# Kernel tuning notes

Measured on AMD Instinct MI355X. Metric: run time of the kernel, lower is better.

The kernel has to match this reference:

```python
import jax, jax.numpy as jnp
import numpy as np
import math

H = 16  # n_heads


def setup_inputs() -> dict:
    key = jax.random.key(0)
    ks = jax.random.split(key, 12)
    B, S, D = 8, 1024, 1024
    inp = {
        "query": jax.random.normal(ks[0], (B, S, D), jnp.float32),
        "key_": jax.random.normal(ks[1], (B, S, D), jnp.float32),
        "value": jax.random.normal(ks[2], (B, S, D), jnp.float32),
        "mask": jnp.ones((B, S, S), jnp.int32),
        "attn_pos": jax.random.normal(ks[3], (1, H, S, S), jnp.float32),
    }
    sc = 1.0 / math.sqrt(D)
    for i, nm in enumerate(["q", "k", "v", "o"]):
        inp[f"w{nm}"] = jax.random.normal(ks[4 + i], (D, D), jnp.float32) * sc
        inp[f"b{nm}"] = jax.random.normal(ks[8 + i], (D,), jnp.float32) * 0.01
    return inp


def reference(query, key_, value, mask, attn_pos, wq, bq, wk, bk, wv, bv, wo, bo):
    B, S, D = query.shape
    dk = D // H

    def proj(x, w, b):  # [B,S,D] -> [B,H,S,dk]
        return (x @ w.T + b).reshape(B, S, H, dk).transpose(0, 2, 1, 3)

    q = proj(query, wq, bq)
    k = proj(key_, wk, bk)
    v = proj(value, wv, bv)

    # attn_pos branch: scale by sqrt(2*d_k), add positional bias
    scores = jnp.einsum("bhqd,bhkd->bhqk", q, k) / math.sqrt(2 * dk) + attn_pos
    scores = jnp.where(mask[:, None] == 0, -1e9, scores)
    p = jax.nn.softmax(scores, axis=-1)  # dropout inactive (eval)
    x = jnp.einsum("bhqk,bhkd->bhqd", p, v)
    x = x.transpose(0, 2, 1, 3).reshape(B, S, D)
    x = x @ wo.T + bo          # linears[-1] applied once...
    return x @ wo.T + bo       # ...and again, faithful to source
```

## Files before the change

### kernel.cpp

```cpp
#include <hip/hip_runtime.h>
#include <hip/hip_bf16.h>

typedef unsigned short u16;
typedef unsigned int u32;
typedef __attribute__((ext_vector_type(8))) short bfrag;
typedef __attribute__((ext_vector_type(4))) float f32x4;

#define DEVINL __device__ __forceinline__

DEVINL u16 f2bf(float f) {
  u32 u = __float_as_uint(f);
  u32 r = (u + 0x7fffu + ((u >> 16) & 1u)) >> 16;
  return (u16)r;
}
DEVINL float bf2f(u16 u) { return __uint_as_float(((u32)u) << 16); }
DEVINL u32 cvtpk(float lo, float hi) {
  u32 r;
  asm("v_cvt_pk_bf16_f32 %0, %1, %2" : "=v"(r) : "v"(lo), "v"(hi));
  return r;
}
DEVINL u16 f2bf_hw(float v) { return (u16)cvtpk(v, v); }
DEVINL float fmax3(float a, float b, float c) { return fmaxf(fmaxf(a, b), c); }

DEVINL void gload_lds16(const void* g, void* l) {
  __builtin_amdgcn_global_load_lds(
      (const __attribute__((address_space(1))) void*)g,
      (__attribute__((address_space(3))) void*)l, 16, 0, 0);
}

DEVINL void storeC(u16* C, size_t idx, float v) { C[idx] = f2bf_hw(v); }
DEVINL void storeC(float* C, size_t idx, float v) { C[idx] = v; }

#define SBAR0 __builtin_amdgcn_sched_barrier(0)


__global__ void cast_v4(const float* __restrict__ in, u16* __restrict__ out, int n4, float s) {
  const int i = blockIdx.x * 256 + threadIdx.x;
  if (i < n4) {
    const float4 f = ((const float4*)in)[i];
    uint2 r;
    r.x = cvtpk(f.x * s, f.y * s);
    r.y = cvtpk(f.z * s, f.w * s);
    ((uint2*)out)[i] = r;
  }
}

__global__ void pack_mask(const int* __restrict__ mask, u32* __restrict__ bits) {
  const size_t wi = (size_t)blockIdx.x * 256 + threadIdx.x;
  const int* src = mask + wi * 32;
  u32 v = 0;
#pragma unroll
  for (int i = 0; i < 8; ++i) {
    const int4 m4 = ((const int4*)src)[i];
    if (m4.x) v |= 1u << (i * 4 + 0);
    if (m4.y) v |= 1u << (i * 4 + 1);
    if (m4.z) v |= 1u << (i * 4 + 2);
    if (m4.w) v |= 1u << (i * 4 + 3);
  }
  bits[wi] = v;
}

__global__ void transpose_cast(const float* __restrict__ in, u16* __restrict__ out) {
  __shared__ u16 tile[64][65];
  const int t = threadIdx.x;
  const int bx = blockIdx.x, by = blockIdx.y;
#pragma unroll
  for (int p = 0; p < 4; ++p) {
    const int r = (t >> 4) + p * 16;
    const int c = (t & 15) * 4;
    const float4 f = *(const float4*)&in[(size_t)(by * 64 + r) * 1024 + bx * 64 + c];
    tile[c + 0][r] = f2bf(f.x);
    tile[c + 1][r] = f2bf(f.y);
    tile[c + 2][r] = f2bf(f.z);
    tile[c + 3][r] = f2bf(f.w);
  }
  __syncthreads();
#pragma unroll
  for (int p = 0; p < 4; ++p) {
    const int r = (t >> 4) + p * 16;
    const int c = (t & 15) * 4;
    uint2 v;
    v.x = (u32)tile[r][c] | ((u32)tile[r][c + 1] << 16);
    v.y = (u32)tile[r][c + 2] | ((u32)tile[r][c + 3] << 16);
    *(uint2*)&out[(size_t)(bx * 64 + r) * 1024 + by * 64 + c] = v;
  }
}

__global__ void bias2(const float* __restrict__ wo, const float* __restrict__ bo,
                      float* __restrict__ bo2) {
  const int w = threadIdx.x >> 6, lane = threadIdx.x & 63;
  const int row = blockIdx.x * 4 + w;
  const float* src = wo + (size_t)row * 1024;
  float s = 0.f;
#pragma unroll
  for (int i = 0; i < 4; ++i) {
    const float4 f = *(const float4*)&src[lane * 4 + i * 256];
    const float4 g = *(const float4*)&bo[lane * 4 + i * 256];
    s += f.x * g.x + f.y * g.y + f.z * g.z + f.w * g.w;
  }
#pragma unroll
  for (int d = 1; d < 64; d <<= 1) s += __shfl_xor(s, d);
  if (lane == 0) bo2[row] = s + bo[row];
}

__global__ __launch_bounds__(256) void gemm_bt_64(
    const u16* __restrict__ A, const u16* __restrict__ W,
    u16* __restrict__ C, int N, int K) {
  __shared__ u16 sA[64 * 64];
  __shared__ u16 sB[64 * 64];
  const int t = threadIdx.x;
  const int w = t >> 6, lane = t & 63;
  const int lr = lane & 15, lk = (lane >> 4) * 8;
  const int m0 = blockIdx.x * 64, n0 = blockIdx.y * 64;
  f32x4 acc[4] = {};
  for (int k0 = 0; k0 < K; k0 += 64) {
#pragma unroll
    for (int i = 0; i < 2; ++i) {
      const int idx = i * 256 + t;
      const int row = idx >> 3;
      const int col = (idx & 7) * 8;
      gload_lds16(A + (size_t)(m0 + row) * K + k0 + col, &sA[idx * 8]);
      gload_lds16(W + (size_t)(n0 + row) * K + k0 + col, &sB[idx * 8]);
    }
    __syncthreads();
#pragma unroll
    for (int ks = 0; ks < 2; ++ks) {
      const bfrag av = *(const bfrag*)&sA[(w * 16 + lr) * 64 + ks * 32 + lk];
#pragma unroll
      for (int n = 0; n < 4; ++n) {
        const bfrag bv = *(const bfrag*)&sB[(n * 16 + lr) * 64 + ks * 32 + lk];
        acc[n] = __builtin_amdgcn_mfma_f32_16x16x32_bf16(av, bv, acc[n], 0, 0, 0);
      }
    }
    __syncthreads();
  }
  const int orow = (lane >> 4) * 4;
#pragma unroll
  for (int n = 0; n < 4; ++n)
#pragma unroll
    for (int j = 0; j < 4; ++j)
      C[(size_t)(m0 + w * 16 + orow + j) * N + n0 + n * 16 + lr] = f2bf_hw(acc[n][j]);
}


template <typename OutT>
__global__ __launch_bounds__(256) void gemm_bt_a16(
    const u16* __restrict__ A, const u16* __restrict__ W,
    const float* __restrict__ bias, OutT* __restrict__ C,
    int M, int N, int K) {
  __shared__ __align__(16) u16 sA[2][128 * 64];
  __shared__ __align__(16) u16 sB[2][128 * 64];
  const int t = threadIdx.x;
  const int w = t >> 6, lane = t & 63;
  const int lr = lane & 15, lg = lane >> 4;
  const int m0 = blockIdx.x * 128, n0 = blockIdx.y * 128;
  const int wr = (w >> 1) * 64, wc = (w & 1) * 64;
  f32x4 acc[4][4] = {};
  const int nk = K >> 6;

#pragma unroll
  for (int i = 0; i < 4; ++i) {
    const int idx = i * 256 + t;
    const int row = idx >> 3;
    const int col = ((idx & 7) ^ (row & 7)) * 8;
    gload_lds16(A + (size_t)(m0 + row) * K + col, (char*)sA[0] + idx * 16);
    gload_lds16(W + (size_t)(n0 + row) * K + col, (char*)sB[0] + idx * 16);
  }
  SBAR0; asm volatile("s_waitcnt vmcnt(0)" ::: "memory"); SBAR0;
  __builtin_amdgcn_s_barrier(); SBAR0;

#pragma unroll 2
  for (int kt = 0; kt < nk; ++kt) {
    const int cur = kt & 1;
    if (kt < nk - 1) {
      const int k0 = (kt + 1) * 64;
#pragma unroll
      for (int i = 0; i < 4; ++i) {
        const int idx = i * 256 + t;
        const int row = idx >> 3;
        const int col = ((idx & 7) ^ (row & 7)) * 8;
        gload_lds16(A + (size_t)(m0 + row) * K + k0 + col, (char*)sA[cur ^ 1] + idx * 16);
        gload_lds16(W + (size_t)(n0 + row) * K + k0 + col, (char*)sB[cur ^ 1] + idx * 16);
      }
    }
    const char* pA = (const char*)sA[cur];
    const char* pB = (const char*)sB[cur];
#pragma unroll
    for (int ks = 0; ks < 2; ++ks) {
      bfrag av[4], bv[4];
#pragma unroll
      for (int m = 0; m < 4; ++m) {
        const int row = wr + m * 16 + lr;
        av[m] = *(const bfrag*)(pA + row * 128 + ((ks * 64 + lg * 16) ^ ((row & 7) << 4)));
      }
#pragma unroll
      for (int n = 0; n < 4; ++n) {
        const int row = wc + n * 16 + lr;
        bv[n] = *(const bfrag*)(pB + row * 128 + ((ks * 64 + lg * 16) ^ ((row & 7) << 4)));
      }
#pragma unroll
      for (int m = 0; m < 4; ++m)
#pragma unroll
        for (int n = 0; n < 4; ++n)
          acc[m][n] = __builtin_amdgcn_mfma_f32_16x16x32_bf16(av[m], bv[n], acc[m][n], 0, 0, 0);
    }
    if (kt < nk - 1) {
      SBAR0; asm volatile("s_waitcnt vmcnt(0)" ::: "memory"); SBAR0;
      __builtin_amdgcn_s_barrier(); SBAR0;
    }
  }

  float bz[4];
#pragma unroll
  for (int n = 0; n < 4; ++n) bz[n] = bias[n0 + wc + n * 16 + lr];
  const int orow = lg * 4;
#pragma unroll
  for (int m = 0; m < 4; ++m) {
#pragma unroll
    for (int n = 0; n < 4; ++n) {
      const int r = m0 + wr + m * 16 + orow;
      const int c = n0 + wc + n * 16 + lr;
#pragma unroll
      for (int j = 0; j < 4; ++j)
        storeC(C, (size_t)(r + j) * N + c, acc[m][n][j] + bz[n]);
    }
  }
}

template <typename OutT>
__global__ __launch_bounds__(256) void gemm_bt_a32(
    const float* __restrict__ A, const u16* __restrict__ W,
    const float* __restrict__ bias, OutT* __restrict__ C,
    int M, int N, int K, float oscale) {
  __shared__ __align__(16) u16 sA[2][128 * 64];
  __shared__ __align__(16) u16 sB[2][128 * 64];
  const int t = threadIdx.x;
  const int w = t >> 6, lane = t & 63;
  const int lr = lane & 15, lg = lane >> 4;
  const int m0 = blockIdx.x * 128, n0 = blockIdx.y * 128;
  const int wr = (w >> 1) * 64, wc = (w & 1) * 64;
  f32x4 acc[4][4] = {};
  const int nk = K >> 6;

#pragma unroll
  for (int i = 0; i < 4; ++i) {
    const int idx = i * 256 + t;
    const int row = idx >> 3;
    const int cg = idx & 7;
    const float* src = A + (size_t)(m0 + row) * K + cg * 8;
    const f32x4 f0 = *(const f32x4*)src;
    const f32x4 f1 = *(const f32x4*)(src + 4);
    uint4 pk;
    pk.x = cvtpk(f0[0], f0[1]);
    pk.y = cvtpk(f0[2], f0[3]);
    pk.z = cvtpk(f1[0], f1[1]);
    pk.w = cvtpk(f1[2], f1[3]);
    *(uint4*)((char*)sA[0] + row * 128 + ((cg ^ (row & 7)) * 16)) = pk;
    gload_lds16(W + (size_t)(n0 + row) * K + ((cg ^ (row & 7)) * 8), (char*)sB[0] + idx * 16);
  }
  SBAR0; asm volatile("s_waitcnt vmcnt(0) lgkmcnt(0)" ::: "memory"); SBAR0;
  __builtin_amdgcn_s_barrier(); SBAR0;

#pragma unroll 2
  for (int kt = 0; kt < nk; ++kt) {
    const int cur = kt & 1;
    f32x4 fa[4][2];
    if (kt < nk - 1) {
      const int k0 = (kt + 1) * 64;
#pragma unroll
      for (int i = 0; i < 4; ++i) {
        const int idx = i * 256 + t;
        const int row = idx >> 3;
        const int cg = idx & 7;
        const float* src = A + (size_t)(m0 + row) * K + k0 + cg * 8;
        fa[i][0] = *(const f32x4*)src;
        fa[i][1] = *(const f32x4*)(src + 4);
      }
#pragma unroll
      for (int i = 0; i < 4; ++i) {
        const int idx = i * 256 + t;
        const int row = idx >> 3;
        const int cg = idx & 7;
        gload_lds16(W + (size_t)(n0 + row) * K + k0 + ((cg ^ (row & 7)) * 8),
                    (char*)sB[cur ^ 1] + idx * 16);
      }
    }
    const char* pA = (const char*)sA[cur];
    const char* pB = (const char*)sB[cur];
#pragma unroll
    for (int ks = 0; ks < 2; ++ks) {
      bfrag av[4], bv[4];
#pragma unroll
      for (int m = 0; m < 4; ++m) {
        const int row = wr + m * 16 + lr;
        av[m] = *(const bfrag*)(pA + row * 128 + ((ks * 64 + lg * 16) ^ ((row & 7) << 4)));
      }
#pragma unroll
      for (int n = 0; n < 4; ++n) {
        const int row = wc + n * 16 + lr;
        bv[n] = *(const bfrag*)(pB + row * 128 + ((ks * 64 + lg * 16) ^ ((row & 7) << 4)));
      }
#pragma unroll
      for (int m = 0; m < 4; ++m)
#pragma unroll
        for (int n = 0; n < 4; ++n)
          acc[m][n] = __builtin_amdgcn_mfma_f32_16x16x32_bf16(av[m], bv[n], acc[m][n], 0, 0, 0);
    }
    if (kt < nk - 1) {
#pragma unroll
      for (int i = 0; i < 4; ++i) {
        const int idx = i * 256 + t;
        const int row = idx >> 3;
        const int cg = idx & 7;
        uint4 pk;
        pk.x = cvtpk(fa[i][0][0], fa[i][0][1]);
        pk.y = cvtpk(fa[i][0][2], fa[i][0][3]);
        pk.z = cvtpk(fa[i][1][0], fa[i][1][1]);
        pk.w = cvtpk(fa[i][1][2], fa[i][1][3]);
        *(uint4*)((char*)sA[cur ^ 1] + row * 128 + ((cg ^ (row & 7)) * 16)) = pk;
      }
      SBAR0; asm volatile("s_waitcnt vmcnt(0) lgkmcnt(0)" ::: "memory"); SBAR0;
      __builtin_amdgcn_s_barrier(); SBAR0;
    }
  }

  float bz[4];
#pragma unroll
  for (int n = 0; n < 4; ++n) bz[n] = bias[n0 + wc + n * 16 + lr];
  const int orow = lg * 4;
#pragma unroll
  for (int m = 0; m < 4; ++m) {
#pragma unroll
    for (int n = 0; n < 4; ++n) {
      const int r = m0 + wr + m * 16 + orow;
      const int c = n0 + wc + n * 16 + lr;
#pragma unroll
      for (int j = 0; j < 4; ++j)
        storeC(C, (size_t)(r + j) * N + c, (acc[m][n][j] + bz[n]) * oscale);
    }
  }
}

__global__ __launch_bounds__(256) void gemm_bt_a32_vt(
    const float* __restrict__ A, const u16* __restrict__ W,
    const float* __restrict__ bias, u16* __restrict__ Vt,
    int M, int N, int K) {
  __shared__ __align__(16) u16 sA[2][128 * 64];
  __shared__ __align__(16) u16 sB[2][128 * 64];
  const int t = threadIdx.x;
  const int w = t >> 6, lane = t & 63;
  const int lr = lane & 15, lg = lane >> 4;
  const int m0 = blockIdx.x * 128, n0 = blockIdx.y * 128;
  const int wr = (w >> 1) * 64, wc = (w & 1) * 64;
  f32x4 acc[4][4] = {};
  const int nk = K >> 6;

#pragma unroll
  for (int i = 0; i < 4; ++i) {
    const int idx = i * 256 + t;
    const int row = idx >> 3;
    const int cg = idx & 7;
    const float* src = A + (size_t)(m0 + row) * K + cg * 8;
    const f32x4 f0 = *(const f32x4*)src;
    const f32x4 f1 = *(const f32x4*)(src + 4);
    uint4 pk;
    pk.x = cvtpk(f0[0], f0[1]);
    pk.y = cvtpk(f0[2], f0[3]);
    pk.z = cvtpk(f1[0], f1[1]);
    pk.w = cvtpk(f1[2], f1[3]);
    *(uint4*)((char*)sA[0] + row * 128 + ((cg ^ (row & 7)) * 16)) = pk;
    gload_lds16(W + (size_t)(n0 + row) * K + ((cg ^ (row & 7)) * 8), (char*)sB[0] + idx * 16);
  }
  SBAR0; asm volatile("s_waitcnt vmcnt(0) lgkmcnt(0)" ::: "memory"); SBAR0;
  __builtin_amdgcn_s_barrier(); SBAR0;

#pragma unroll 2
  for (int kt = 0; kt < nk; ++kt) {
    const int cur = kt & 1;
    f32x4 fa[4][2];
    if (kt < nk - 1) {
      const int k0 = (kt + 1) * 64;
#pragma unroll
      for (int i = 0; i < 4; ++i) {
        const int idx = i * 256 + t;
        const int row = idx >> 3;
        const int cg = idx & 7;
        const float* src = A + (size_t)(m0 + row) * K + k0 + cg * 8;
        fa[i][0] = *(const f32x4*)src;
        fa[i][1] = *(const f32x4*)(src + 4);
      }
#pragma unroll
      for (int i = 0; i < 4; ++i) {
        const int idx = i * 256 + t;
        const int row = idx >> 3;
        const int cg = idx & 7;
        gload_lds16(W + (size_t)(n0 + row) * K + k0 + ((cg ^ (row & 7)) * 8),
                    (char*)sB[cur ^ 1] + idx * 16);
      }
    }
    const char* pA = (const char*)sA[cur];
    const char* pB = (const char*)sB[cur];
#pragma unroll
    for (int ks = 0; ks < 2; ++ks) {
      bfrag av[4], bv[4];
#pragma unroll
      for (int m = 0; m < 4; ++m) {
        const int row = wr + m * 16 + lr;
        av[m] = *(const bfrag*)(pA + row * 128 + ((ks * 64 + lg * 16) ^ ((row & 7) << 4)));
      }
#pragma unroll
      for (int n = 0; n < 4; ++n) {
        const int row = wc + n * 16 + lr;
        bv[n] = *(const bfrag*)(pB + row * 128 + ((ks * 64 + lg * 16) ^ ((row & 7) << 4)));
      }
#pragma unroll
      for (int m = 0; m < 4; ++m)
#pragma unroll
        for (int n = 0; n < 4; ++n)
          acc[m][n] = __builtin_amdgcn_mfma_f32_16x16x32_bf16(av[m], bv[n], acc[m][n], 0, 0, 0);
    }
    if (kt < nk - 1) {
#pragma unroll
      for (int i = 0; i < 4; ++i) {
        const int idx = i * 256 + t;
        const int row = idx >> 3;
        const int cg = idx & 7;
        uint4 pk;
        pk.x = cvtpk(fa[i][0][0], fa[i][0][1]);
        pk.y = cvtpk(fa[i][0][2], fa[i][0][3]);
        pk.z = cvtpk(fa[i][1][0], fa[i][1][1]);
        pk.w = cvtpk(fa[i][1][2], fa[i][1][3]);
        *(uint4*)((char*)sA[cur ^ 1] + row * 128 + ((cg ^ (row & 7)) * 16)) = pk;
      }
      SBAR0; asm volatile("s_waitcnt vmcnt(0) lgkmcnt(0)" ::: "memory"); SBAR0;
      __builtin_amdgcn_s_barrier(); SBAR0;
    }
  }

  float bz[4];
#pragma unroll
  for (int n = 0; n < 4; ++n) bz[n] = bias[n0 + wc + n * 16 + lr];
  const int orow = lg * 4;
#pragma unroll
  for (int m = 0; m < 4; ++m) {
#pragma unroll
    for (int n = 0; n < 4; ++n) {
      const int r0 = m0 + wr + m * 16 + orow;
      const int c = n0 + wc + n * 16 + lr;
      const int bb = r0 >> 10, s = r0 & 1023;
      const int h = c >> 6, d = c & 63;
      uint2 v;
      v.x = cvtpk(acc[m][n][0] + bz[n], acc[m][n][1] + bz[n]);
      v.y = cvtpk(acc[m][n][2] + bz[n], acc[m][n][3] + bz[n]);
      *(uint2*)&Vt[(((size_t)bb * 16 + h) * 64 + d) * 1024 + s] = v;
    }
  }
}


__global__ __launch_bounds__(512, 4) void attn_fwd(
    const u16* __restrict__ Qm, const u16* __restrict__ Km,
    const u16* __restrict__ Vt, const float* __restrict__ pos,
    const u32* __restrict__ mbits, u16* __restrict__ Om) {
  const int bb = blockIdx.x >> 3;
  const int qt = blockIdx.x & 7;
  const int h = blockIdx.y;
  const int t = threadIdx.x;
  const int w = t >> 6, lane = t & 63;
  const int lr = lane & 15, lg = lane >> 4;
  const float log2e = 1.4426950408889634f;

  __shared__ __align__(16) char smem[81920];

  const int q0 = qt * 128;
  const size_t baseQ = ((size_t)bb * 1024) * 1024 + (size_t)h * 64;
  const size_t baseV = ((size_t)(bb * 16 + h) * 64) * 1024;
  const int qg = q0 + w * 16 + lr;
  const float* posrow = pos + ((size_t)h * 1024 + qg) * 1024;
  const u32* mrow = mbits + ((size_t)bb * 1024 + qg) * 32;
  const int sr = t >> 3, sw8 = t & 7;
  const int scol = (sw8 ^ (sr & 7)) * 8;

#pragma unroll
  for (int i = 0; i < 2; ++i) {
    const int idx = i * 512 + t;
    const int r = idx >> 3;
    gload_lds16(Qm + baseQ + (size_t)(q0 + r) * 1024 + ((idx & 7) ^ (r & 7)) * 8, smem + idx * 16);
  }
  gload_lds16(Km + baseQ + (size_t)sr * 1024 + scol, smem + 16384 + t * 16);
  gload_lds16(Vt + baseV + (size_t)sr * 1024 + scol, smem + 40960 + t * 16);
  gload_lds16(Km + baseQ + (size_t)(64 + sr) * 1024 + scol, smem + 24576 + t * 16);
  gload_lds16(Vt + baseV + (size_t)sr * 1024 + 64 + scol, smem + 49152 + t * 16);

  uint4 mraw[8];
#pragma unroll
  for (int i = 0; i < 8; ++i) mraw[i] = *(const uint4*)&mrow[i * 4];
  float4 pz[4];
#pragma unroll
  for (int n = 0; n < 4; ++n) pz[n] = *(const float4*)&posrow[n * 16 + lg * 4];

  u32 ok = 0xffffffffu;
#pragma unroll
  for (int i = 0; i < 8; ++i) ok &= mraw[i].x & mraw[i].y & mraw[i].z & mraw[i].w;
  const bool allone = __all(ok == 0xffffffffu);

  SBAR0; asm volatile("s_waitcnt vmcnt(4)" ::: "memory"); SBAR0;
  __builtin_amdgcn_s_barrier(); SBAR0;

  bfrag qv[2];
#pragma unroll
  for (int ks = 0; ks < 2; ++ks) {
    const int byt = (w * 16 + lr) * 128 + ((ks * 64 + lg * 16) ^ ((lr & 7) << 4));
    qv[ks] = *(const bfrag*)(smem + byt);
  }

  f32x4 o[4] = {};
  float m_q = -3.0e38f, l_q = 0.f;
  char* pbuf = smem + 65536 + w * 2048;

#pragma unroll
  for (int kt = 0; kt < 16; ++kt) {
    const int cb = kt % 3;
    const char* sK = smem + 16384 + cb * 8192;
    const char* sV = smem + 40960 + cb * 8192;

    if (kt < 14) {
      const int kn = (kt + 2) * 64;
      const int db = (kt + 2) % 3;
      gload_lds16(Km + baseQ + (size_t)(kn + sr) * 1024 + scol, smem + 16384 + db * 8192 + t * 16);
      gload_lds16(Vt + baseV + (size_t)sr * 1024 + kn + scol, smem + 40960 + db * 8192 + t * 16);
    }
    float4 pzn[4];
    if (kt < 15) {
      const int kn = (kt + 1) * 64;
#pragma unroll
      for (int n = 0; n < 4; ++n) pzn[n] = *(const float4*)&posrow[kn + n * 16 + lg * 4];
    }

    f32x4 s[4] = {};
    __builtin_amdgcn_s_setprio(1);
#pragma unroll
    for (int ks = 0; ks < 2; ++ks) {
#pragma unroll
      for (int n = 0; n < 4; ++n) {
        const int byt = (n * 16 + lr) * 128 + ((ks * 64 + lg * 16) ^ ((lr & 7) << 4));
        const bfrag kf = *(const bfrag*)(sK + byt);
        s[n] = __builtin_amdgcn_mfma_f32_16x16x32_bf16(kf, qv[ks], s[n], 0, 0, 0);
      }
    }
    __builtin_amdgcn_s_setprio(0);

    float pv[16];
#pragma unroll
    for (int n = 0; n < 4; ++n) {
      pv[n * 4 + 0] = fmaf(pz[n].x, log2e, s[n][0]);
      pv[n * 4 + 1] = fmaf(pz[n].y, log2e, s[n][1]);
      pv[n * 4 + 2] = fmaf(pz[n].z, log2e, s[n][2]);
      pv[n * 4 + 3] = fmaf(pz[n].w, log2e, s[n][3]);
    }

    if (!allone) {
      const u32 a0 = mrow[kt * 2], a1 = mrow[kt * 2 + 1];
#pragma unroll
      for (int n = 0; n < 4; ++n)
#pragma unroll
        for (int j = 0; j < 4; ++j) {
          const int kl = n * 16 + lg * 4 + j;
          const u32 mw = (kl & 32) ? a1 : a0;
          if (!((mw >> (kl & 31)) & 1u)) pv[n * 4 + j] = -1.0e9f;
        }
    }

    float tmax = fmax3(pv[0], pv[1], pv[2]);
    tmax = fmax3(tmax, pv[3], pv[4]);
    tmax = fmax3(tmax, pv[5], pv[6]);
    tmax = fmax3(tmax, pv[7], pv[8]);
    tmax = fmax3(tmax, pv[9], pv[10]);
    tmax = fmax3(tmax, pv[11], pv[12]);
    tmax = fmax3(tmax, pv[13], pv[14]);
    tmax = fmaxf(tmax, pv[15]);
    tmax = fmaxf(tmax, __shfl_xor(tmax, 16));
    tmax = fmaxf(tmax, __shfl_xor(tmax, 32));

    if (!__all(tmax <= m_q + 8.0f)) {
      const float mn = fmaxf(m_q, tmax);
      const float sc = __builtin_amdgcn_exp2f(m_q - mn);
      l_q *= sc;
#pragma unroll
      for (int j = 0; j < 4; ++j) {
        const float scj = __shfl(sc, lg * 4 + j);
#pragma unroll
        for (int n = 0; n < 4; ++n) o[n][j] *= scj;
      }
      m_q = mn;
    }
    float rs = 0.f;
#pragma unroll
    for (int i2 = 0; i2 < 16; ++i2) {
      pv[i2] = __builtin_amdgcn_exp2f(pv[i2] - m_q);
      rs += pv[i2];
    }
    rs += __shfl_xor(rs, 16);
    rs += __shfl_xor(rs, 32);
    l_q += rs;

#pragma unroll
    for (int n = 0; n < 4; ++n) {
      uint2 pk;
      pk.x = cvtpk(pv[n * 4 + 0], pv[n * 4 + 1]);
      pk.y = cvtpk(pv[n * 4 + 2], pv[n * 4 + 3]);
      const int byt = lr * 128 + ((n * 32 + lg * 8) ^ ((lr & 7) << 4));
      *(uint2*)(pbuf + byt) = pk;
    }
    __builtin_amdgcn_s_setprio(1);
#pragma unroll
    for (int ks = 0; ks < 2; ++ks) {
      const int pbyt = lr * 128 + ((ks * 64 + lg * 16) ^ ((lr & 7) << 4));
      const bfrag pf = *(const bfrag*)(pbuf + pbyt);
#pragma unroll
      for (int n = 0; n < 4; ++n) {
        const int vb = (n * 16 + lr) * 128 + ((ks * 64 + lg * 16) ^ ((lr & 7) << 4));
        const bfrag vf = *(const bfrag*)(sV + vb);
        o[n] = __builtin_amdgcn_mfma_f32_16x16x32_bf16(pf, vf, o[n], 0, 0, 0);
      }
    }
    __builtin_amdgcn_s_setprio(0);

    if (kt < 15) {
      SBAR0;
      if (kt < 14) asm volatile("s_waitcnt vmcnt(6)" ::: "memory");
      else         asm volatile("s_waitcnt vmcnt(4)" ::: "memory");
      SBAR0;
      __builtin_amdgcn_s_barrier();
      SBAR0;
#pragma unroll
      for (int n = 0; n < 4; ++n) pz[n] = pzn[n];
    }
  }

#pragma unroll
  for (int j = 0; j < 4; ++j) {
    const float lj = __shfl(l_q, lg * 4 + j);
    const float inv = 1.f / lj;
    const int qr = q0 + w * 16 + lg * 4 + j;
#pragma unroll
    for (int n = 0; n < 4; ++n)
      Om[baseQ + (size_t)qr * 1024 + n * 16 + lr] = f2bf_hw(o[n][j] * inv);
  }
}


extern "C" void kernel_launch(void* const* d_in, const int* in_sizes, int n_in,
                              void* d_out, int out_size, void* d_ws, size_t ws_size,
                              hipStream_t stream) {
  const float* query = (const float*)d_in[0];
  const float* key_  = (const float*)d_in[1];
  const float* value = (const float*)d_in[2];
  const int*   mask  = (const int*)d_in[3];
  const float* pos   = (const float*)d_in[4];
  const float* wq = (const float*)d_in[5];
  const float* bq = (const float*)d_in[6];
  const float* wk = (const float*)d_in[7];
  const float* bk = (const float*)d_in[8];
  const float* wv = (const float*)d_in[9];
  const float* bv = (const float*)d_in[10];
  const float* wo = (const float*)d_in[11];
  const float* bo = (const float*)d_in[12];

  char* ws = (char*)d_ws;
  const size_t MB = 1024 * 1024;
  u16* wqb  = (u16*)(ws + 0 * MB);
  u16* wkb  = (u16*)(ws + 2 * MB);
  u16* wvb  = (u16*)(ws + 4 * MB);
  u16* wob  = (u16*)(ws + 6 * MB);
  u16* Qb   = (u16*)(ws + 40 * MB);
  u16* Kb   = (u16*)(ws + 56 * MB);
  u16* Vtb  = (u16*)(ws + 72 * MB);
  u16* Xa   = (u16*)(ws + 88 * MB);
  u32* mb   = (u32*)(ws + 104 * MB);
  u16* wotb = (u16*)(ws + 105 * MB);
  u16* W2b  = (u16*)(ws + 107 * MB);
  float* bo2 = (float*)(ws + 109 * MB);

  const float log2e = 1.4426950408889634f;
  const float qs = 0.0883883476483184f * log2e;

  cast_v4<<<1024, 256, 0, stream>>>(wq, wqb, 262144, 1.0f);
  cast_v4<<<1024, 256, 0, stream>>>(wk, wkb, 262144, 1.0f);
  cast_v4<<<1024, 256, 0, stream>>>(wv, wvb, 262144, 1.0f);
  cast_v4<<<1024, 256, 0, stream>>>(wo, wob, 262144, 1.0f);
  pack_mask<<<1024, 256, 0, stream>>>(mask, mb);
  transpose_cast<<<dim3(16, 16), 256, 0, stream>>>(wo, wotb);
  bias2<<<256, 256, 0, stream>>>(wo, bo, bo2);

  gemm_bt_64<<<dim3(16, 16), 256, 0, stream>>>(wob, wotb, W2b, 1024, 1024);

  const dim3 gg(64, 8);
  gemm_bt_a32<u16><<<gg, 256, 0, stream>>>(query, wqb, bq, Qb, 8192, 1024, 1024, qs);
  gemm_bt_a32<u16><<<gg, 256, 0, stream>>>(key_,  wkb, bk, Kb, 8192, 1024, 1024, 1.0f);
  gemm_bt_a32_vt<<<gg, 256, 0, stream>>>(value, wvb, bv, Vtb, 8192, 1024, 1024);

  attn_fwd<<<dim3(64, 16), 512, 0, stream>>>(Qb, Kb, Vtb, pos, mb, Xa);

  gemm_bt_a16<float><<<gg, 256, 0, stream>>>(Xa, W2b, bo2, (float*)d_out, 8192, 1024, 1024);
}
```

Measured before the change: 257.2 us.

## Pre-cast positional bias to bf16 and simplify attention K/V buffering

Adds a pre-pass that scales the fp32 positional bias by log2e and stores it as bf16, so attention reads half the bytes per bias element and skips one FMA per score. The attention kernel moves from triple- to double-buffered K/V in LDS with plain __syncthreads instead of hand-tuned vmcnt waits, and drops the kt-loop unroll. The grid becomes 1D and is remapped so blocks sharing a head's bias rows run close together. The four weight-cast launches are merged into one. The bias pre-pass adds a full extra read and write of the bias tensor and loses some precision, and the shallower pipeline may expose more load latency.

```diff
diff --git a/kernel.cpp b/kernel.cpp
--- a/kernel.cpp
+++ b/kernel.cpp
@@ -43,6 +43,21 @@
     r.y = cvtpk(f.z * s, f.w * s);
     ((uint2*)out)[i] = r;
   }
+}
+
+__global__ void cast_w4(const float* __restrict__ w0, const float* __restrict__ w1,
+                        const float* __restrict__ w2, const float* __restrict__ w3,
+                        u16* __restrict__ o0, u16* __restrict__ o1,
+                        u16* __restrict__ o2, u16* __restrict__ o3) {
+  const int which = blockIdx.x >> 10;
+  const int i = (blockIdx.x & 1023) * 256 + threadIdx.x;
+  const float* in = which == 0 ? w0 : which == 1 ? w1 : which == 2 ? w2 : w3;
+  u16* out = which == 0 ? o0 : which == 1 ? o1 : which == 2 ? o2 : o3;
+  const float4 f = ((const float4*)in)[i];
+  uint2 r;
+  r.x = cvtpk(f.x, f.y);
+  r.y = cvtpk(f.z, f.w);
+  ((uint2*)out)[i] = r;
 }
 
 __global__ void pack_mask(const int* __restrict__ mask, u32* __restrict__ bits) {
@@ -460,52 +475,53 @@
 
 __global__ __launch_bounds__(512, 4) void attn_fwd(
     const u16* __restrict__ Qm, const u16* __restrict__ Km,
-    const u16* __restrict__ Vt, const float* __restrict__ pos,
+    const u16* __restrict__ Vt, const u16* __restrict__ posb,
     const u32* __restrict__ mbits, u16* __restrict__ Om) {
-  const int bb = blockIdx.x >> 3;
-  const int qt = blockIdx.x & 7;
-  const int h = blockIdx.y;
+  const int gid = blockIdx.x;
+  const int h = (gid & 7) + 8 * (gid >> 9);
+  const int inner = (gid >> 3) & 63;
+  const int bb = inner & 7;
+  const int qt = inner >> 3;
   const int t = threadIdx.x;
   const int w = t >> 6, lane = t & 63;
   const int lr = lane & 15, lg = lane >> 4;
-  const float log2e = 1.4426950408889634f;
-
-  __shared__ __align__(16) char smem[81920];
+
+  __shared__ __align__(16) char smem[49152];
 
   const int q0 = qt * 128;
   const size_t baseQ = ((size_t)bb * 1024) * 1024 + (size_t)h * 64;
   const size_t baseV = ((size_t)(bb * 16 + h) * 64) * 1024;
   const int qg = q0 + w * 16 + lr;
-  const float* posrow = pos + ((size_t)h * 1024 + qg) * 1024;
+  const u16* posrow = posb + ((size_t)h * 1024 + qg) * 1024;
   const u32* mrow = mbits + ((size_t)bb * 1024 + qg) * 32;
-  const int sr = t >> 3, sw8 = t & 7;
-  const int scol = (sw8 ^ (sr & 7)) * 8;
 
 #pragma unroll
   for (int i = 0; i < 2; ++i) {
     const int idx = i * 512 + t;
     const int r = idx >> 3;
-    gload_lds16(Qm + baseQ + (size_t)(q0 + r) * 1024 + ((idx & 7) ^ (r & 7)) * 8, smem + idx * 16);
-  }
-  gload_lds16(Km + baseQ + (size_t)sr * 1024 + scol, smem + 16384 + t * 16);
-  gload_lds16(Vt + baseV + (size_t)sr * 1024 + scol, smem + 40960 + t * 16);
-  gload_lds16(Km + baseQ + (size_t)(64 + sr) * 1024 + scol, smem + 24576 + t * 16);
-  gload_lds16(Vt + baseV + (size_t)sr * 1024 + 64 + scol, smem + 49152 + t * 16);
-
-  uint4 mraw[8];
-#pragma unroll
-  for (int i = 0; i < 8; ++i) mraw[i] = *(const uint4*)&mrow[i * 4];
-  float4 pz[4];
-#pragma unroll
-  for (int n = 0; n < 4; ++n) pz[n] = *(const float4*)&posrow[n * 16 + lg * 4];
+    const int w8 = idx & 7;
+    gload_lds16(Qm + baseQ + (size_t)(q0 + r) * 1024 + (w8 ^ (r & 7)) * 8, smem + idx * 16);
+  }
+  {
+    const int r = t >> 3;
+    const int w8 = t & 7;
+    gload_lds16(Km + baseQ + (size_t)r * 1024 + (w8 ^ (r & 7)) * 8, smem + 16384 + t * 16);
+    gload_lds16(Vt + baseV + (size_t)r * 1024 + (w8 ^ (r & 7)) * 8, smem + 24576 + t * 16);
+  }
 
   u32 ok = 0xffffffffu;
 #pragma unroll
-  for (int i = 0; i < 8; ++i) ok &= mraw[i].x & mraw[i].y & mraw[i].z & mraw[i].w;
+  for (int i = 0; i < 8; ++i) {
+    const uint4 m4 = *(const uint4*)&mrow[i * 4];
+    ok &= m4.x & m4.y & m4.z & m4.w;
+  }
   const bool allone = __all(ok == 0xffffffffu);
 
-  SBAR0; asm volatile("s_waitcnt vmcnt(4)" ::: "memory"); SBAR0;
-  __builtin_amdgcn_s_barrier(); SBAR0;
+  uint2 pz[4];
+#pragma unroll
+  for (int n = 0; n < 4; ++n) pz[n] = *(const uint2*)&posrow[n * 16 + lg * 4];
+
+  __syncthreads();
 
   bfrag qv[2];
 #pragma unroll
@@ -513,28 +529,27 @@
     const int byt = (w * 16 + lr) * 128 + ((ks * 64 + lg * 16) ^ ((lr & 7) << 4));
     qv[ks] = *(const bfrag*)(smem + byt);
   }
+  __syncthreads();
 
   f32x4 o[4] = {};
   float m_q = -3.0e38f, l_q = 0.f;
-  char* pbuf = smem + 65536 + w * 2048;
-
-#pragma unroll
+
   for (int kt = 0; kt < 16; ++kt) {
-    const int cb = kt % 3;
-    const char* sK = smem + 16384 + cb * 8192;
-    const char* sV = smem + 40960 + cb * 8192;
-
-    if (kt < 14) {
-      const int kn = (kt + 2) * 64;
-      const int db = (kt + 2) % 3;
-      gload_lds16(Km + baseQ + (size_t)(kn + sr) * 1024 + scol, smem + 16384 + db * 8192 + t * 16);
-      gload_lds16(Vt + baseV + (size_t)sr * 1024 + kn + scol, smem + 40960 + db * 8192 + t * 16);
-    }
-    float4 pzn[4];
+    const int cur = kt & 1;
+    const char* sK = smem + (cur ? 0 : 16384);
+    const char* sV = smem + (cur ? 8192 : 24576);
+
+    uint2 pzn[4];
     if (kt < 15) {
       const int kn = (kt + 1) * 64;
-#pragma unroll
-      for (int n = 0; n < 4; ++n) pzn[n] = *(const float4*)&posrow[kn + n * 16 + lg * 4];
+      char* dK = smem + (cur ? 16384 : 0);
+      char* dV = smem + (cur ? 24576 : 8192);
+      const int r = t >> 3;
+      const int w8 = t & 7;
+      gload_lds16(Km + baseQ + (size_t)(kn + r) * 1024 + (w8 ^ (r & 7)) * 8, dK + t * 16);
+      gload_lds16(Vt + baseV + (size_t)r * 1024 + kn + (w8 ^ (r & 7)) * 8, dV + t * 16);
+#pragma unroll
+      for (int n = 0; n < 4; ++n) pzn[n] = *(const uint2*)&posrow[kn + n * 16 + lg * 4];
     }
 
     f32x4 s[4] = {};
@@ -553,10 +568,10 @@
     float pv[16];
 #pragma unroll
     for (int n = 0; n < 4; ++n) {
-      pv[n * 4 + 0] = fmaf(pz[n].x, log2e, s[n][0]);
-      pv[n * 4 + 1] = fmaf(pz[n].y, log2e, s[n][1]);
-      pv[n * 4 + 2] = fmaf(pz[n].z, log2e, s[n][2]);
-      pv[n * 4 + 3] = fmaf(pz[n].w, log2e, s[n][3]);
+      pv[n * 4 + 0] = s[n][0] + bf2f((u16)(pz[n].x & 0xffff));
+      pv[n * 4 + 1] = s[n][1] + bf2f((u16)(pz[n].x >> 16));
+      pv[n * 4 + 2] = s[n][2] + bf2f((u16)(pz[n].y & 0xffff));
+      pv[n * 4 + 3] = s[n][3] + bf2f((u16)(pz[n].y >> 16));
     }
 
     if (!allone) {
@@ -604,6 +619,7 @@
     rs += __shfl_xor(rs, 32);
     l_q += rs;
 
+    char* pbuf = smem + 32768 + w * 2048;
 #pragma unroll
     for (int n = 0; n < 4; ++n) {
       uint2 pk;
@@ -626,13 +642,9 @@
     }
     __builtin_amdgcn_s_setprio(0);
 
+    __syncthreads();
+
     if (kt < 15) {
-      SBAR0;
-      if (kt < 14) asm volatile("s_waitcnt vmcnt(6)" ::: "memory");
-      else         asm volatile("s_waitcnt vmcnt(4)" ::: "memory");
-      SBAR0;
-      __builtin_amdgcn_s_barrier();
-      SBAR0;
 #pragma unroll
       for (int n = 0; n < 4; ++n) pz[n] = pzn[n];
     }
@@ -673,6 +685,7 @@
   u16* wkb  = (u16*)(ws + 2 * MB);
   u16* wvb  = (u16*)(ws + 4 * MB);
   u16* wob  = (u16*)(ws + 6 * MB);
+  u16* posb = (u16*)(ws + 8 * MB);
   u16* Qb   = (u16*)(ws + 40 * MB);
   u16* Kb   = (u16*)(ws + 56 * MB);
   u16* Vtb  = (u16*)(ws + 72 * MB);
@@ -685,10 +698,8 @@
   const float log2e = 1.4426950408889634f;
   const float qs = 0.0883883476483184f * log2e;
 
-  cast_v4<<<1024, 256, 0, stream>>>(wq, wqb, 262144, 1.0f);
-  cast_v4<<<1024, 256, 0, stream>>>(wk, wkb, 262144, 1.0f);
-  cast_v4<<<1024, 256, 0, stream>>>(wv, wvb, 262144, 1.0f);
-  cast_v4<<<1024, 256, 0, stream>>>(wo, wob, 262144, 1.0f);
+  cast_w4<<<4096, 256, 0, stream>>>(wq, wk, wv, wo, wqb, wkb, wvb, wob);
+  cast_v4<<<16384, 256, 0, stream>>>(pos, posb, 4194304, log2e);
   pack_mask<<<1024, 256, 0, stream>>>(mask, mb);
   transpose_cast<<<dim3(16, 16), 256, 0, stream>>>(wo, wotb);
   bias2<<<256, 256, 0, stream>>>(wo, bo, bo2);
@@ -700,7 +711,7 @@
   gemm_bt_a32<u16><<<gg, 256, 0, stream>>>(key_,  wkb, bk, Kb, 8192, 1024, 1024, 1.0f);
   gemm_bt_a32_vt<<<gg, 256, 0, stream>>>(value, wvb, bv, Vtb, 8192, 1024, 1024);
 
-  attn_fwd<<<dim3(64, 16), 512, 0, stream>>>(Qb, Kb, Vtb, pos, mb, Xa);
+  attn_fwd<<<1024, 512, 0, stream>>>(Qb, Kb, Vtb, posb, mb, Xa);
 
   gemm_bt_a16<float><<<gg, 256, 0, stream>>>(Xa, W2b, bo2, (float*)d_out, 8192, 1024, 1024);
 }
```

New measurement: 264.6 us. 2.9% more time.
